# Kernel optimization log

Measured on AMD Instinct MI355X. Metric: run time of the kernel, lower is better.

## Reference

```python
import jax, jax.numpy as jnp
import numpy as np

D_MODEL = 1024
NUM_HEADS = 16
HEAD_DIM = D_MODEL // NUM_HEADS

def _trunc_normal(key, shape, std=0.02, a=-0.04, b=0.04):
    u = jax.random.truncated_normal(key, a / std, b / std, shape, dtype=jnp.float32)
    return u * std

def setup_inputs() -> dict:
    key = jax.random.key(0)
    kx, kq, kk, kv, ko = jax.random.split(key, 5)
    x = jax.random.normal(kx, (4, 2048, D_MODEL), dtype=jnp.float32)
    Wq = _trunc_normal(kq, (D_MODEL, D_MODEL))
    Wk = _trunc_normal(kk, (D_MODEL, D_MODEL))
    Wv = _trunc_normal(kv, (D_MODEL, D_MODEL))
    Wo = _trunc_normal(ko, (D_MODEL, D_MODEL))
    return {"x": x, "Wq": Wq, "Wk": Wk, "Wv": Wv, "Wo": Wo}

def reference(x, Wq, Wk, Wv, Wo):
    B, S, D = x.shape
    H, Dh = NUM_HEADS, HEAD_DIM
    # projections: x @ W.T
    Q = jnp.einsum('bsd,ed->bse', x, Wq).reshape(B, S, H, Dh).transpose(0, 2, 1, 3)
    K = jnp.einsum('bsd,ed->bse', x, Wk).reshape(B, S, H, Dh).transpose(0, 2, 1, 3)
    V = jnp.einsum('bsd,ed->bse', x, Wv).reshape(B, S, H, Dh).transpose(0, 2, 1, 3)
    scale = 1.0 / jnp.sqrt(jnp.asarray(Dh, dtype=x.dtype))
    scores = jnp.einsum('bhqd,bhkd->bhqk', Q, K) * scale  # [B,H,S,S]
    causal = jnp.tril(jnp.ones((S, S), dtype=bool))  # True where attend allowed
    scores = jnp.where(causal, scores, -jnp.inf)
    attn = jax.nn.softmax(scores, axis=-1)
    ctx = jnp.einsum('bhqk,bhkd->bhqd', attn, V)  # [B,H,S,Dh]
    ctx = ctx.transpose(0, 2, 1, 3).reshape(B, S, D)
    out = jnp.einsum('bsd,ed->bse', ctx, Wo)
    return out
```

## Files before the change

### kernel.cpp

```cpp
#include <hip/hip_runtime.h>

#define D_MODEL 1024
#define SEQ 2048
#define BATCH 4
#define HEADS 16
#define HDIM 64

typedef short bf16x8 __attribute__((ext_vector_type(8)));
typedef float f32x4 __attribute__((ext_vector_type(4)));

#define FENCE() asm volatile("" ::: "memory")

__device__ __forceinline__ unsigned short f2bf(float f) {
  union { float f; unsigned int u; } c; c.f = f;
  unsigned int u = c.u;
  unsigned int r = (u + 0x7FFFu + ((u >> 16) & 1u)) >> 16;
  return (unsigned short)r;
}

__device__ __forceinline__ unsigned int cvt_pk_bf16(float a, float b) {
  unsigned int r;
  asm("v_cvt_pk_bf16_f32 %0, %1, %2" : "=v"(r) : "v"(a), "v"(b));
  return r;
}

__device__ __forceinline__ float exp2_hw(float x) {
  float r;
  asm("v_exp_f32 %0, %1" : "=v"(r) : "v"(x));
  return r;
}

__device__ __forceinline__ void async16(const void* g, const void* lds) {
  __builtin_amdgcn_global_load_lds((const __attribute__((address_space(1))) void*)g,
                                   (__attribute__((address_space(3))) void*)lds, 16, 0, 0);
}

__global__ void cvt_all(const float* __restrict__ x,
                        const float* __restrict__ Wq, const float* __restrict__ Wk,
                        const float* __restrict__ Wv, const float* __restrict__ Wo,
                        unsigned short* __restrict__ xb,
                        unsigned short* __restrict__ Wqkv,
                        unsigned short* __restrict__ Wob) {
  int bid = blockIdx.x;
  const float* s;
  unsigned short* d;
  int i;
  if (bid < 8192) {
    s = x; d = xb; i = bid * 256 + threadIdx.x;
  } else {
    int b = (bid - 8192) >> 10;
    i = ((bid - 8192) & 1023) * 256 + threadIdx.x;
    s = (b == 0) ? Wq : (b == 1) ? Wk : (b == 2) ? Wv : Wo;
    d = (b == 3) ? Wob : (Wqkv + b * (D_MODEL * D_MODEL));
  }
  float4 v = ((const float4*)s)[i];
  ushort4 o;
  o.x = f2bf(v.x); o.y = f2bf(v.y); o.z = f2bf(v.z); o.w = f2bf(v.w);
  ((ushort4*)d)[i] = o;
}

__global__ __launch_bounds__(512, 2) void gemm256qk(
    const unsigned short* __restrict__ A, const unsigned short* __restrict__ Bw,
    unsigned short* __restrict__ Qd, unsigned short* __restrict__ Kd) {
  __shared__ unsigned short At[2][256 * 64];
  __shared__ unsigned short Bt[2][256 * 64];
  const int t = threadIdx.x;
  const int lane = t & 63;
  const int wid = t >> 6;
  const int wm = wid >> 2;
  const int wn = wid & 3;

  const int gx = gridDim.x;
  const int nwg = gridDim.x * gridDim.y;
  int flat = blockIdx.y * gx + blockIdx.x;
  flat = (flat & 7) * (nwg >> 3) + (flat >> 3);
  const int m0 = (flat / gx) * 256;
  const int n0 = (flat % gx) * 256;

  const int K = 1024;
  f32x4 acc[8][4] = {};

  const int srow = t >> 3;
  const int scol = ((t & 7) ^ (srow & 7)) << 3;
  const unsigned short* Ags = A + (size_t)(m0 + srow) * K + scol;
  const unsigned short* Bgs = Bw + (size_t)(n0 + srow) * K + scol;

  const int l15 = lane & 15;
  const int lh = lane >> 4;
  const int rsw = (l15 & 7) << 4;
  const int cb0 = (lh * 16) ^ rsw;
  const int cb1 = (64 + lh * 16) ^ rsw;
  const int aBase = (wm * 128 + l15) * 128;
  const int bBase = (wn * 64 + l15) * 128;

#define STG_A(o, c, kn) async16(Ags + (size_t)(c) * 64 * K + (kn), &At[o][(c) * 4096 + t * 8])
#define STG_B(o, c, kn) async16(Bgs + (size_t)(c) * 64 * K + (kn), &Bt[o][(c) * 4096 + t * 8])

  STG_B(0, 0, 0); STG_B(0, 1, 0); STG_B(0, 2, 0); STG_B(0, 3, 0);
  STG_A(0, 0, 0); STG_A(0, 1, 0); STG_A(0, 2, 0); STG_A(0, 3, 0);
  asm volatile("s_waitcnt vmcnt(0)" ::: "memory");
  __builtin_amdgcn_s_barrier();
  FENCE();

  for (int kt = 0; kt < K; kt += 64) {
    const int s = (kt >> 6) & 1;
    const int o = s ^ 1;
    const int kn = kt + 64;
    const bool more = kn < K;
    const char* Ab = (const char*)&At[s][0];
    const char* Bb = (const char*)&Bt[s][0];

    bf16x8 bfr[4][2];
#pragma unroll
    for (int p = 0; p < 4; ++p) {
      bf16x8 af[2][2];
#pragma unroll
      for (int i = 0; i < 2; ++i) {
        af[i][0] = *(const bf16x8*)(Ab + aBase + (2 * p + i) * 2048 + cb0);
        af[i][1] = *(const bf16x8*)(Ab + aBase + (2 * p + i) * 2048 + cb1);
      }
      if (p == 0) {
#pragma unroll
        for (int fn = 0; fn < 4; ++fn) {
          bfr[fn][0] = *(const bf16x8*)(Bb + bBase + fn * 2048 + cb0);
          bfr[fn][1] = *(const bf16x8*)(Bb + bBase + fn * 2048 + cb1);
        }
        if (more) { STG_B(o, 0, kn); STG_B(o, 1, kn); }
      } else if (p == 1) {
        if (more) { STG_B(o, 2, kn); STG_B(o, 3, kn); }
      } else if (p == 2) {
        if (more) { STG_A(o, 0, kn); STG_A(o, 2, kn); }
      } else {
        if (more) { STG_A(o, 1, kn); STG_A(o, 3, kn); }
      }
      __builtin_amdgcn_s_barrier();
      FENCE();
      __builtin_amdgcn_s_setprio(1);
#pragma unroll
      for (int ks = 0; ks < 2; ++ks)
#pragma unroll
        for (int i = 0; i < 2; ++i)
#pragma unroll
          for (int fn = 0; fn < 4; ++fn)
            acc[2 * p + i][fn] = __builtin_amdgcn_mfma_f32_16x16x32_bf16(
                af[i][ks], bfr[fn][ks], acc[2 * p + i][fn], 0, 0, 0);
      __builtin_amdgcn_s_setprio(0);
      FENCE();
      if (p == 1) {
        if (more) asm volatile("s_waitcnt vmcnt(4)" ::: "memory");
        else      asm volatile("s_waitcnt vmcnt(0)" ::: "memory");
      } else if (p == 3) {
        if (more) asm volatile("s_waitcnt vmcnt(2)" ::: "memory");
        else      asm volatile("s_waitcnt vmcnt(0)" ::: "memory");
      }
      __builtin_amdgcn_s_barrier();
      FENCE();
    }
  }
#undef STG_A
#undef STG_B

#pragma unroll
  for (int fm = 0; fm < 8; ++fm) {
#pragma unroll
    for (int fn = 0; fn < 4; ++fn) {
#pragma unroll
      for (int r = 0; r < 4; ++r) {
        float v = acc[fm][fn][r];
        int m = m0 + wm * 128 + fm * 16 + lh * 4 + r;
        int n = n0 + wn * 64 + fn * 16 + l15;
        int p = n >> 10;
        int h = (n >> 6) & 15;
        int dh = n & 63;
        int b = m >> 11;
        int sx = m & 2047;
        unsigned short* dst = (p == 0) ? Qd : Kd;
        if (p == 0) v *= 0.18033688011112042f;
        dst[(((size_t)(b * HEADS + h)) * SEQ + sx) * HDIM + dh] = f2bf(v);
      }
    }
  }
}

template <int MODE>
__global__ __launch_bounds__(512, 1) void gemm128(
    const unsigned short* __restrict__ A, const unsigned short* __restrict__ Bw,
    int nOfs, unsigned short* __restrict__ Vtd, float* __restrict__ Od) {
  __shared__ unsigned short At[2][128 * 64];
  __shared__ unsigned short Bt[2][256 * 64];
  const int t = threadIdx.x;
  const int lane = t & 63;
  const int wid = t >> 6;
  const int wm = wid >> 1;
  const int wn = wid & 1;

  const int gx = gridDim.x;
  const int nwg = gridDim.x * gridDim.y;
  int flat = blockIdx.y * gx + blockIdx.x;
  flat = (flat & 7) * (nwg >> 3) + (flat >> 3);
  const int m0 = (flat / gx) * 128;
  const int n0 = nOfs + (flat % gx) * 256;

  const int K = 1024;
  f32x4 acc[2][8] = {};

  const int srow = t >> 3;
  const int scol = ((t & 7) ^ (srow & 7)) << 3;
  const unsigned short* Ags = A + (size_t)(m0 + srow) * K + scol;
  const unsigned short* Bgs = Bw + (size_t)(n0 + srow) * K + scol;

  const int l15 = lane & 15;
  const int lh = lane >> 4;
  const int rsw = (l15 & 7) << 4;
  const int cb0 = (lh * 16) ^ rsw;
  const int cb1 = (64 + lh * 16) ^ rsw;
  const int aBase = (wm * 32 + l15) * 128;
  const int bBase = (wn * 128 + l15) * 128;

#define STG_A(o, c, kn) async16(Ags + (size_t)(c) * 64 * K + (kn), &At[o][(c) * 4096 + t * 8])
#define STG_B(o, c, kn) async16(Bgs + (size_t)(c) * 64 * K + (kn), &Bt[o][(c) * 4096 + t * 8])

  STG_A(0, 0, 0); STG_A(0, 1, 0); STG_B(0, 0, 0); STG_B(0, 2, 0);
  STG_B(0, 1, 0); STG_B(0, 3, 0);
  asm volatile("s_waitcnt vmcnt(0)" ::: "memory");
  __builtin_amdgcn_s_barrier();
  FENCE();

  for (int kt = 0; kt < K; kt += 64) {
    const int s = (kt >> 6) & 1;
    const int o = s ^ 1;
    const int kn = kt + 64;
    const bool more = kn < K;
    const char* Ab = (const char*)&At[s][0];
    const char* Bb = (const char*)&Bt[s][0];

    bf16x8 af[2][2];
#pragma unroll
    for (int p = 0; p < 4; ++p) {
      if (p == 0) {
#pragma unroll
        for (int i = 0; i < 2; ++i) {
          af[i][0] = *(const bf16x8*)(Ab + aBase + i * 2048 + cb0);
          af[i][1] = *(const bf16x8*)(Ab + aBase + i * 2048 + cb1);
        }
      }
      bf16x8 bfr[2][2];
#pragma unroll
      for (int j = 0; j < 2; ++j) {
        bfr[j][0] = *(const bf16x8*)(Bb + bBase + (2 * p + j) * 2048 + cb0);
        bfr[j][1] = *(const bf16x8*)(Bb + bBase + (2 * p + j) * 2048 + cb1);
      }
      if (p == 0)      { if (more) { STG_A(o, 0, kn); STG_A(o, 1, kn); } }
      else if (p == 1) { if (more) { STG_B(o, 0, kn); STG_B(o, 2, kn); } }
      else if (p == 2) { if (more) { STG_B(o, 1, kn); STG_B(o, 3, kn); } }
      __builtin_amdgcn_s_barrier();
      FENCE();
      __builtin_amdgcn_s_setprio(1);
#pragma unroll
      for (int ks = 0; ks < 2; ++ks)
#pragma unroll
        for (int i = 0; i < 2; ++i)
#pragma unroll
          for (int j = 0; j < 2; ++j) {
            if (MODE == 1)
              acc[i][2 * p + j] = __builtin_amdgcn_mfma_f32_16x16x32_bf16(
                  bfr[j][ks], af[i][ks], acc[i][2 * p + j], 0, 0, 0);
            else
              acc[i][2 * p + j] = __builtin_amdgcn_mfma_f32_16x16x32_bf16(
                  af[i][ks], bfr[j][ks], acc[i][2 * p + j], 0, 0, 0);
          }
      __builtin_amdgcn_s_setprio(0);
      FENCE();
      if (p == 1) {
        if (more) asm volatile("s_waitcnt vmcnt(4)" ::: "memory");
        else      asm volatile("s_waitcnt vmcnt(0)" ::: "memory");
      } else if (p == 3) {
        if (more) asm volatile("s_waitcnt vmcnt(2)" ::: "memory");
        else      asm volatile("s_waitcnt vmcnt(0)" ::: "memory");
      }
      __builtin_amdgcn_s_barrier();
      FENCE();
    }
  }
#undef STG_A
#undef STG_B

#pragma unroll
  for (int fm = 0; fm < 2; ++fm) {
#pragma unroll
    for (int fn = 0; fn < 8; ++fn) {
#pragma unroll
      for (int r = 0; r < 4; ++r) {
        float v = acc[fm][fn][r];
        if (MODE == 1) {
          int n = n0 + wn * 128 + fn * 16 + lh * 4 + r;
          int m = m0 + wm * 32 + fm * 16 + l15;
          int h = (n >> 6) & 15;
          int d = n & 63;
          int b = m >> 11;
          int s = m & 2047;
          Vtd[(((size_t)(b * HEADS + h)) * HDIM + d) * SEQ + s] = f2bf(v);
        } else {
          int m = m0 + wm * 32 + fm * 16 + lh * 4 + r;
          int n = n0 + wn * 128 + fn * 16 + l15;
          Od[(size_t)m * D_MODEL + n] = v;
        }
      }
    }
  }
}

__global__ __launch_bounds__(256, 3) void attn_fwd(
    const unsigned short* __restrict__ Qg, const unsigned short* __restrict__ Kg,
    const unsigned short* __restrict__ Vtg, unsigned short* __restrict__ Cg) {
  __shared__ unsigned short Kl[64 * 64];
  __shared__ unsigned short Vl[64 * 64];
  __shared__ unsigned short Pl[4][32 * 72];
  char* KlB = (char*)Kl;
  char* VlB = (char*)Vl;

  const int t = threadIdx.x;
  const int lane = t & 63;
  const int wq = t >> 6;
  const int bh = blockIdx.x;
  const int q0 = (15 - blockIdx.y) * 128;
  const size_t base = (size_t)bh * SEQ * HDIM;
  const unsigned short* Qb = Qg + base;
  const unsigned short* Kb = Kg + base;
  const unsigned short* Vb = Vtg + base;
  char* PlB = (char*)&Pl[wq][0];

  const int l15 = lane & 15;
  const int lh = lane >> 4;
  const int qrow = q0 + wq * 32;

  bf16x8 qf[2][2];
#pragma unroll
  for (int fm = 0; fm < 2; ++fm)
#pragma unroll
    for (int ks = 0; ks < 2; ++ks)
      qf[fm][ks] = *(const bf16x8*)&Qb[(size_t)(qrow + fm * 16 + l15) * HDIM +
                                       ks * 32 + lh * 8];

  f32x4 acc[2][4] = {};
  float lrun[2] = {0.f, 0.f};

  const int srow = t >> 3;
  const int sc8 = ((t & 7) ^ (srow & 7)) << 3;

  const int kv_end = q0 + 128;
  for (int kv0 = 0; kv0 < kv_end; kv0 += 64) {
    __syncthreads();
    async16(Kb + (size_t)(kv0 + srow) * HDIM + sc8, &Kl[t * 8]);
    async16(Kb + (size_t)(kv0 + 32 + srow) * HDIM + sc8, &Kl[2048 + t * 8]);
    async16(Vb + (size_t)srow * SEQ + kv0 + sc8, &Vl[t * 8]);
    async16(Vb + (size_t)(32 + srow) * SEQ + kv0 + sc8, &Vl[2048 + t * 8]);
    asm volatile("s_waitcnt vmcnt(0)" ::: "memory");
    __syncthreads();

    if (kv0 <= qrow + 31) {
      f32x4 sfr[2][4] = {};
#pragma unroll
      for (int ks = 0; ks < 2; ++ks) {
        bf16x8 kf[4];
#pragma unroll
        for (int fn = 0; fn < 4; ++fn) {
          int row = fn * 16 + l15;
          kf[fn] = *(const bf16x8*)&KlB[row * 128 +
                                        ((ks * 64 + lh * 16) ^ ((row & 7) << 4))];
        }
#pragma unroll
        for (int fm = 0; fm < 2; ++fm)
#pragma unroll
          for (int fn = 0; fn < 4; ++fn)
            sfr[fm][fn] = __builtin_amdgcn_mfma_f32_16x16x32_bf16(
                kf[fn], qf[fm][ks], sfr[fm][fn], 0, 0, 0);
      }

      const bool need_mask = (kv0 + 63) > qrow;
#pragma unroll
      for (int fm = 0; fm < 2; ++fm) {
        const int q = qrow + fm * 16 + l15;
        float p[4][4];
#pragma unroll
        for (int fn = 0; fn < 4; ++fn)
#pragma unroll
          for (int r = 0; r < 4; ++r) p[fn][r] = sfr[fm][fn][r];
        if (need_mask) {
#pragma unroll
          for (int fn = 0; fn < 4; ++fn)
#pragma unroll
            for (int r = 0; r < 4; ++r) {
              int key = kv0 + fn * 16 + lh * 4 + r;
              if (key > q) p[fn][r] = -1e30f;
            }
        }
        float st = 0.f;
#pragma unroll
        for (int fn = 0; fn < 4; ++fn)
#pragma unroll
          for (int r = 0; r < 4; ++r) {
            p[fn][r] = exp2_hw(p[fn][r]);
            st += p[fn][r];
          }
        st += __shfl_xor(st, 16);
        st += __shfl_xor(st, 32);
        lrun[fm] += st;

#pragma unroll
        for (int fn = 0; fn < 4; ++fn) {
#pragma unroll
          for (int w = 0; w < 2; ++w) {
            unsigned int pk = cvt_pk_bf16(p[fn][2 * w], p[fn][2 * w + 1]);
            *(unsigned int*)&PlB[(fm * 16 + l15) * 144 + fn * 32 + lh * 8 + w * 4] = pk;
          }
        }
      }

#pragma unroll
      for (int ks = 0; ks < 2; ++ks) {
        bf16x8 pf[2], vf[4];
#pragma unroll
        for (int fm = 0; fm < 2; ++fm)
          pf[fm] = *(const bf16x8*)&PlB[(fm * 16 + l15) * 144 + ks * 64 + lh * 16];
#pragma unroll
        for (int fn = 0; fn < 4; ++fn) {
          int row = fn * 16 + l15;
          vf[fn] = *(const bf16x8*)&VlB[row * 128 +
                                        ((ks * 64 + lh * 16) ^ ((row & 7) << 4))];
        }
#pragma unroll
        for (int fm = 0; fm < 2; ++fm)
#pragma unroll
          for (int fn = 0; fn < 4; ++fn)
            acc[fm][fn] = __builtin_amdgcn_mfma_f32_16x16x32_bf16(
                pf[fm], vf[fn], acc[fm][fn], 0, 0, 0);
      }
    }
  }

  const int b = bh >> 4;
  const int h = bh & 15;
#pragma unroll
  for (int fm = 0; fm < 2; ++fm) {
    float inv = 1.0f / lrun[fm];
    float ivr[4];
#pragma unroll
    for (int r = 0; r < 4; ++r) ivr[r] = __shfl(inv, lh * 4 + r);
#pragma unroll
    for (int r = 0; r < 4; ++r) {
      int s = qrow + fm * 16 + lh * 4 + r;
#pragma unroll
      for (int fn = 0; fn < 4; ++fn) {
        int dh = fn * 16 + l15;
        Cg[((size_t)(b * SEQ + s)) * D_MODEL + h * HDIM + dh] =
            f2bf(acc[fm][fn][r] * ivr[r]);
      }
    }
  }
}

extern "C" void kernel_launch(void* const* d_in, const int* in_sizes, int n_in,
                              void* d_out, int out_size, void* d_ws, size_t ws_size,
                              hipStream_t stream) {
  const float* x = (const float*)d_in[0];
  const float* Wq = (const float*)d_in[1];
  const float* Wk = (const float*)d_in[2];
  const float* Wv = (const float*)d_in[3];
  const float* Wo = (const float*)d_in[4];
  float* out = (float*)d_out;

  char* ws = (char*)d_ws;
  unsigned short* xb   = (unsigned short*)(ws);
  unsigned short* Wqkv = (unsigned short*)(ws + (16u << 20));
  unsigned short* Wob  = (unsigned short*)(ws + (22u << 20));
  unsigned short* Qb   = (unsigned short*)(ws + (24u << 20));
  unsigned short* Kb   = (unsigned short*)(ws + (40u << 20));
  unsigned short* Vtb  = (unsigned short*)(ws + (56u << 20));
  unsigned short* Cb   = (unsigned short*)(ws + (72u << 20));

  cvt_all<<<dim3(12288), dim3(256), 0, stream>>>(x, Wq, Wk, Wv, Wo, xb, Wqkv, Wob);

  gemm256qk<<<dim3(8, 32), dim3(512), 0, stream>>>(xb, Wqkv, Qb, Kb);
  gemm128<1><<<dim3(4, 64), dim3(512), 0, stream>>>(xb, Wqkv, 2048, Vtb, nullptr);
  attn_fwd<<<dim3(64, 16), dim3(256), 0, stream>>>(Qb, Kb, Vtb, Cb);
  gemm128<0><<<dim3(4, 64), dim3(512), 0, stream>>>(Cb, Wob, 0, nullptr, out);
}
```

Before: 154.2 us.

## Stage 128-key K/V tiles per barrier and defer row-sum reduction

The attention kernel now loads 128 keys of K and V into LDS per iteration and processes them as two 64-key halves, halving the number of barrier/wait rounds per block. The cross-lane row-sum shuffles move out of the inner loop, so each lane keeps a partial sum that is reduced once at the end. The cost is double the LDS per block (K and V tiles grow to 16KB each), which may reduce occupancy, plus some wasted loads on the diagonal tile.

```diff
diff --git a/kernel.cpp b/kernel.cpp
--- a/kernel.cpp
+++ b/kernel.cpp
@@ -313,8 +313,8 @@
 __global__ __launch_bounds__(256, 3) void attn_fwd(
     const unsigned short* __restrict__ Qg, const unsigned short* __restrict__ Kg,
     const unsigned short* __restrict__ Vtg, unsigned short* __restrict__ Cg) {
-  __shared__ unsigned short Kl[64 * 64];
-  __shared__ unsigned short Vl[64 * 64];
+  __shared__ unsigned short Kl[128 * 64];
+  __shared__ unsigned short Vl[64 * 128];
   __shared__ unsigned short Pl[4][32 * 72];
   char* KlB = (char*)Kl;
   char* VlB = (char*)Vl;
@@ -343,29 +343,37 @@
                                        ks * 32 + lh * 8];
 
   f32x4 acc[2][4] = {};
-  float lrun[2] = {0.f, 0.f};
+  float lpart[2] = {0.f, 0.f};
 
   const int srow = t >> 3;
   const int sc8 = ((t & 7) ^ (srow & 7)) << 3;
+  const int srowV = t >> 4;
+  const int scV8 = (((t & 15) ^ (srowV & 7)) << 3);
 
   const int kv_end = q0 + 128;
-  for (int kv0 = 0; kv0 < kv_end; kv0 += 64) {
+  for (int kvb = 0; kvb < kv_end; kvb += 128) {
     __syncthreads();
-    async16(Kb + (size_t)(kv0 + srow) * HDIM + sc8, &Kl[t * 8]);
-    async16(Kb + (size_t)(kv0 + 32 + srow) * HDIM + sc8, &Kl[2048 + t * 8]);
-    async16(Vb + (size_t)srow * SEQ + kv0 + sc8, &Vl[t * 8]);
-    async16(Vb + (size_t)(32 + srow) * SEQ + kv0 + sc8, &Vl[2048 + t * 8]);
+#pragma unroll
+    for (int i = 0; i < 4; ++i)
+      async16(Kb + (size_t)(kvb + i * 32 + srow) * HDIM + sc8, &Kl[i * 2048 + t * 8]);
+#pragma unroll
+    for (int i = 0; i < 4; ++i)
+      async16(Vb + (size_t)(i * 16 + srowV) * SEQ + kvb + scV8, &Vl[i * 2048 + t * 8]);
     asm volatile("s_waitcnt vmcnt(0)" ::: "memory");
     __syncthreads();
 
-    if (kv0 <= qrow + 31) {
+#pragma unroll
+    for (int kh = 0; kh < 2; ++kh) {
+      const int kv0 = kvb + kh * 64;
+      if (kv0 > qrow + 31) continue;
+
       f32x4 sfr[2][4] = {};
 #pragma unroll
       for (int ks = 0; ks < 2; ++ks) {
         bf16x8 kf[4];
 #pragma unroll
         for (int fn = 0; fn < 4; ++fn) {
-          int row = fn * 16 + l15;
+          int row = kh * 64 + fn * 16 + l15;
           kf[fn] = *(const bf16x8*)&KlB[row * 128 +
                                         ((ks * 64 + lh * 16) ^ ((row & 7) << 4))];
         }
@@ -403,9 +411,7 @@
             p[fn][r] = exp2_hw(p[fn][r]);
             st += p[fn][r];
           }
-        st += __shfl_xor(st, 16);
-        st += __shfl_xor(st, 32);
-        lrun[fm] += st;
+        lpart[fm] += st;
 
 #pragma unroll
         for (int fn = 0; fn < 4; ++fn) {
@@ -426,8 +432,8 @@
 #pragma unroll
         for (int fn = 0; fn < 4; ++fn) {
           int row = fn * 16 + l15;
-          vf[fn] = *(const bf16x8*)&VlB[row * 128 +
-                                        ((ks * 64 + lh * 16) ^ ((row & 7) << 4))];
+          vf[fn] = *(const bf16x8*)&VlB[row * 256 +
+                                        ((kh * 128 + ks * 64 + lh * 16) ^ ((row & 7) << 4))];
         }
 #pragma unroll
         for (int fm = 0; fm < 2; ++fm)
@@ -443,7 +449,10 @@
   const int h = bh & 15;
 #pragma unroll
   for (int fm = 0; fm < 2; ++fm) {
-    float inv = 1.0f / lrun[fm];
+    float lt = lpart[fm];
+    lt += __shfl_xor(lt, 16);
+    lt += __shfl_xor(lt, 32);
+    float inv = 1.0f / lt;
     float ivr[4];
 #pragma unroll
     for (int r = 0; r < 4; ++r) ivr[r] = __shfl(inv, lh * 4 + r);
```

Result: no change. 151.9 us (median of 3 runs) (-1.4%).
